# Kernel tuning notes

Hardware: AMD Instinct MI355X
Metric: run time of the kernel (lower is better)

## Reference

```python
import jax, jax.numpy as jnp
import numpy as np

EMG_SAMPLE_RATE = 2000
ROLLOUT_FREQ = 50
LEFT_CTX = 32
RIGHT_CTX = 32
NUM_POSITION_STEPS = 2000  # in EMG samples
OUT_CH = 20


def _interp_linear(x, size, align_corners):
    """x: [..., L] -> [..., size]; matches torch F.interpolate(mode='linear')."""
    L = x.shape[-1]
    if align_corners:
        src = jnp.arange(size, dtype=jnp.float32) * ((L - 1) / max(size - 1, 1))
    else:
        src = (jnp.arange(size, dtype=jnp.float32) + 0.5) * (L / size) - 0.5
        src = jnp.clip(src, 0.0, L - 1)
    lo = jnp.floor(src).astype(jnp.int32)
    hi = jnp.minimum(lo + 1, L - 1)
    w = (src - lo.astype(jnp.float32)).astype(x.dtype)
    return x[..., lo] * (1 - w) + x[..., hi] * w


def setup_inputs() -> dict:
    key = jax.random.key(0)
    ks = jax.random.split(key, 8)
    B, C, T = 32, 16, 8000
    F, K, H = 512, 65, 512
    emg = jax.random.normal(ks[0], (B, C, T), jnp.float32)
    joint_angles = jax.random.normal(ks[1], (B, OUT_CH, T), jnp.float32)
    no_ik_failure = jnp.ones((B, T), dtype=bool)
    conv_w = jax.random.normal(ks[2], (F, C, K), jnp.float32) * 0.05
    conv_b = jnp.zeros((F,), jnp.float32)
    w1 = jax.random.normal(ks[3], (F + OUT_CH, H), jnp.float32) * 0.04
    b1 = jnp.zeros((H,), jnp.float32)
    w2 = jax.random.normal(ks[4], (H, 2 * OUT_CH), jnp.float32) * 0.04
    b2 = jnp.zeros((2 * OUT_CH,), jnp.float32)
    return dict(emg=emg, joint_angles=joint_angles, no_ik_failure=no_ik_failure,
                provide_initial_pos=1, conv_w=conv_w, conv_b=conv_b,
                w1=w1, b1=b1, w2=w2, b2=b2)


def reference(emg, joint_angles, no_ik_failure, provide_initial_pos,
              conv_w, conv_b, w1, b1, w2, b2):
    B, _, T = emg.shape
    initial_pos = joint_angles[:, :, LEFT_CTX]
    if not provide_initial_pos:
        initial_pos = jnp.zeros_like(initial_pos)

    # encoder: valid Conv1d -> [B, F, T - K + 1] = [B, F, T - 64]
    feats = jax.lax.conv_general_dilated(
        emg, conv_w, window_strides=(1,), padding='VALID',
        dimension_numbers=('NCH', 'OIH', 'NCH')) + conv_b[None, :, None]

    seconds = (T - LEFT_CTX - RIGHT_CTX) / EMG_SAMPLE_RATE
    n_time = round(seconds * ROLLOUT_FREQ)          # static python int
    feats = _interp_linear(feats, n_time, align_corners=True)  # [B, F, n_time]
    num_pos_steps = round(NUM_POSITION_STEPS * (ROLLOUT_FREQ / EMG_SAMPLE_RATE))

    feats_t = jnp.transpose(feats, (2, 0, 1))  # [n_time, B, F]

    def step(prev, inp):
        x_t, t = inp
        # state_condition=True: concat previous pose prediction
        h = jax.nn.relu(jnp.concatenate([x_t, prev], axis=-1) @ w1 + b1)
        out = h @ w2 + b2                       # [B, 2*OUT_CH]
        pos, vel = out[:, :OUT_CH], out[:, OUT_CH:]
        pred = jnp.where(t < num_pos_steps, pos, prev + vel)
        return pred, pred

    _, preds = jax.lax.scan(step, initial_pos,
                            (feats_t, jnp.arange(n_time)))
    pred = jnp.transpose(preds, (1, 2, 0))  # [B, OUT_CH, n_time]

    ja = joint_angles[:, :, LEFT_CTX:T - RIGHT_CTX]
    mask = no_ik_failure[:, LEFT_CTX:T - RIGHT_CTX]
    nt = ja.shape[-1]
    pred_up = _interp_linear(pred, nt, align_corners=False)
    # nearest resample of mask to its own length is identity
    return pred_up, ja, mask
```

## Files before the change

### kernel.cpp

```cpp
#include <hip/hip_runtime.h>

#define NT   198
#define BB   32
#define CC   16
#define TT   8000
#define FF   512
#define KW   65
#define HD   512
#define OUT  20
#define CJ   (CC*KW)
#define KP   1056
#define MM   (NT*BB)
#define TOUT 7936
#define NPS  50

typedef float f4 __attribute__((ext_vector_type(4)));

#define WS_CW 0
#define WS_BX (WS_CW + KP*HD)
#define WS_X  (WS_BX + HD)
#define WS_PR (WS_X  + MM*HD)
#define WS_ET (WS_PR + MM*OUT)
#define WS_W2T (WS_ET + KP*MM)

#define ESPAN 2688
__global__ __launch_bounds__(256) void k_e2(const float* __restrict__ emg,
                                            float* __restrict__ Et) {
    __shared__ float lds_e[ESPAN];
    const int bx = blockIdx.x;
    const int bq = bx >> 4, c = bx & 15;
    const int tc = blockIdx.y;
    const int t0 = tc * 66;
    const int tid = threadIdx.x;
    const float CSTEP = 7935.0f / 197.0f;
    const int elo0 = (int)floorf((float)t0 * CSTEP);
    const float* erow = emg + (size_t)(bq * CC + c) * TT;
    for (int i = tid; i < ESPAN; i += 256) {
        int g = elo0 + i;
        lds_e[i] = erow[(g < TT) ? g : (TT - 1)];
    }
    __syncthreads();
    for (int o = tid; o < 65 * 66; o += 256) {
        int j = o / 66;
        int tl = o - j * 66;
        int t = t0 + tl;
        float src = (float)t * CSTEP;
        float fl = floorf(src);
        int lo = (int)fl;
        float w = src - fl;
        int dhi = (w > 0.f && lo < TOUT - 1) ? 1 : 0;
        int li = lo - elo0 + j;
        float v = (1.0f - w) * lds_e[li] + w * lds_e[li + dhi];
        Et[(size_t)(c * KW + j) * MM + bq * NT + t] = v;
    }
}

__global__ void k_ez(float* __restrict__ Et) {
    int r = CJ + blockIdx.x;
    int col = blockIdx.y * 256 + threadIdx.x;
    if (col < MM) Et[(size_t)r * MM + col] = 0.f;
}

__global__ __launch_bounds__(256) void k_cw2(const float* __restrict__ cwraw,
                                             const float* __restrict__ w1,
                                             float* __restrict__ CW) {
    __shared__ float As[32][68];
    __shared__ float Bs[32][68];
    const int m0 = blockIdx.x * 64;
    const int n0 = blockIdx.y * 64;
    const int tid = threadIdx.x;
    const int tx = tid & 15, ty = tid >> 4;
    const int am = tid & 63;
    const int kb8 = (tid >> 6) * 8;
    const int mrow = m0 + am;
    const int mclamp = mrow < CJ ? mrow : CJ - 1;

    f4 acc[4] = {};
    for (int k0 = 0; k0 < FF; k0 += 32) {
        __syncthreads();
        #pragma unroll
        for (int s = 0; s < 8; ++s)
            As[kb8 + s][am] = cwraw[(size_t)(k0 + kb8 + s) * CJ + mclamp];
        {
            int kb = tid >> 4, c4 = tid & 15;
            *(f4*)&Bs[kb][c4 * 4]      = *(const f4*)(w1 + (size_t)(k0 + kb) * HD + n0 + c4 * 4);
            *(f4*)&Bs[kb + 16][c4 * 4] = *(const f4*)(w1 + (size_t)(k0 + kb + 16) * HD + n0 + c4 * 4);
        }
        __syncthreads();
        #pragma unroll
        for (int kk = 0; kk < 32; ++kk) {
            f4 a = *(f4*)&As[kk][ty * 4];
            f4 bq = *(f4*)&Bs[kk][tx * 4];
            acc[0] += a[0] * bq; acc[1] += a[1] * bq;
            acc[2] += a[2] * bq; acc[3] += a[3] * bq;
        }
    }
    #pragma unroll
    for (int i = 0; i < 4; ++i) {
        int r = m0 + ty * 4 + i;
        if (r < CJ) {
            *(f4*)(CW + (size_t)r * HD + n0 + tx * 4) = acc[i];
        } else if (r < KP) {
            f4 z = {0.f, 0.f, 0.f, 0.f};
            *(f4*)(CW + (size_t)r * HD + n0 + tx * 4) = z;
        }
    }
}

__global__ void k_bx(const float* __restrict__ conv_b, const float* __restrict__ w1,
                     const float* __restrict__ b1, float* __restrict__ bX) {
    int h = threadIdx.x;
    float acc = b1[h];
    for (int f = 0; f < FF; ++f) acc += conv_b[f] * w1[f * HD + h];
    bX[h] = acc;
}

__global__ void k_w2t(const float* __restrict__ w2, float* __restrict__ w2t) {
    int q = blockIdx.x;
    int h = threadIdx.x;
    w2t[(size_t)q * HD + h] = w2[(size_t)h * (2 * OUT) + q];
}

__global__ __launch_bounds__(128) void k_x8(const float* __restrict__ Et,
                                            const float* __restrict__ CW,
                                            const float* __restrict__ bX,
                                            float* __restrict__ X0,
                                            float* __restrict__ X1) {
    __shared__ float As[32][68];
    __shared__ float Bs0[32][68];
    __shared__ float Bs1[32][68];
    const int m0 = blockIdx.x * 64;
    const int n0 = blockIdx.y * 128;
    const int kc = blockIdx.z;
    const int kbase = kc ? 512 : 0;
    const int NK = kc ? 17 : 16;
    const int tid = threadIdx.x;
    const int tm = tid >> 4;
    const int tn = tid & 15;
    const int akr = tid >> 4;
    const int ag  = tid & 15;
    const int bkr = tid >> 5;
    const int bg  = tid & 31;

    f4 acc0[8] = {}, acc1[8] = {};

    for (int kt = 0; kt < NK; ++kt) {
        const int k0 = kbase + kt * 32;
        __syncthreads();
        #pragma unroll
        for (int s = 0; s < 4; ++s) {
            f4 v = *(const f4*)(Et + (size_t)(k0 + akr + 8 * s) * MM + m0 + ag * 4);
            *(f4*)&As[akr + 8 * s][ag * 4] = v;
        }
        #pragma unroll
        for (int s = 0; s < 8; ++s) {
            int kr = bkr + 4 * s;
            f4 v = *(const f4*)(CW + (size_t)(k0 + kr) * HD + n0 + bg * 4);
            if (bg < 16) *(f4*)&Bs0[kr][bg * 4] = v;
            else         *(f4*)&Bs1[kr][(bg - 16) * 4] = v;
        }
        __syncthreads();
        #pragma unroll
        for (int kk = 0; kk < 32; ++kk) {
            f4 a0 = *(const f4*)&As[kk][tm * 8];
            f4 a1 = *(const f4*)&As[kk][tm * 8 + 4];
            f4 b0 = *(const f4*)&Bs0[kk][tn * 4];
            f4 b1 = *(const f4*)&Bs1[kk][tn * 4];
            #pragma unroll
            for (int i = 0; i < 4; ++i) {
                acc0[i]     += a0[i] * b0;  acc1[i]     += a0[i] * b1;
                acc0[i + 4] += a1[i] * b0;  acc1[i + 4] += a1[i] * b1;
            }
        }
    }

    if (kc == 0) {
        f4 bx0 = *(const f4*)(bX + n0 + tn * 4);
        f4 bx1 = *(const f4*)(bX + n0 + 64 + tn * 4);
        #pragma unroll
        for (int i = 0; i < 8; ++i) {
            size_t off = (size_t)(m0 + 8 * tm + i) * HD + n0;
            *(f4*)(X0 + off + tn * 4)      = acc0[i] + bx0;
            *(f4*)(X0 + off + 64 + tn * 4) = acc1[i] + bx1;
        }
    } else {
        #pragma unroll
        for (int i = 0; i < 8; ++i) {
            size_t off = (size_t)(m0 + 8 * tm + i) * HD + n0;
            *(f4*)(X1 + off + tn * 4)      = acc0[i];
            *(f4*)(X1 + off + 64 + tn * 4) = acc1[i];
        }
    }
}

#define DPPADD(x, ctrl) ((x) + __int_as_float(__builtin_amdgcn_mov_dpp(__float_as_int(x), (ctrl), 0xf, 0xf, true)))

#define SCAN_STEP(T, ISPOS) { \
    if (aown) { \
        int tp = (T) + 2; if (tp > NT - 1) tp = NT - 1; \
        float2 xfa = *(const float2*)(Xr0 + (size_t)tp * HD); \
        float2 xfb = *(const float2*)(Xr1 + (size_t)tp * HD); \
        float2 xf; xf.x = xfa.x + xfb.x; xf.y = xfa.y + xfb.y; \
        f4 pp[5]; \
        _Pragma("unroll") \
        for (int g = 0; g < 5; ++g) pp[g] = *(const f4*)&prev_lds[(T) & 1][g * 4]; \
        float h0 = xc.x, h1 = xc.y; \
        _Pragma("unroll") \
        for (int j = 0; j < OUT; ++j) { \
            float pj = pp[j >> 2][j & 3]; \
            h0 = fmaf(pj, w1p[j].x, h0); h1 = fmaf(pj, w1p[j].y, h1); } \
        h0 = fmaxf(h0, 0.f); h1 = fmaxf(h1, 0.f); \
        float2 hw; hw.x = h0; hw.y = h1; \
        *(float2*)&h_lds[(T) & 1][tid >> 4][(2 * tid) & 31] = hw; \
        xc = xn; xn = xf; \
    } \
    __syncthreads(); \
    f4 a = {0.f, 0.f, 0.f, 0.f}; \
    _Pragma("unroll") \
    for (int s = 0; s < 8; ++s) { \
        f4 hv = *(const f4*)&h_lds[(T) & 1][r][s * 4]; \
        a += hv * ((ISPOS) ? wqp[s] : wqv[s]); } \
    float sum = (a[0] + a[1]) + (a[2] + a[3]); \
    sum = DPPADD(sum, 0xB1);    \
    sum = DPPADD(sum, 0x4E);    \
    sum = DPPADD(sum, 0x141);   \
    sum = DPPADD(sum, 0x140);   \
    float outv = sum + ((ISPOS) ? b2p : b2v); \
    myq = (ISPOS) ? outv : (myq + outv); \
    if (r == 0) { \
        predrow[(size_t)(T) * OUT + q] = myq; \
        prev_lds[((T) + 1) & 1][q] = myq; } \
    __syncthreads(); }

__global__ __launch_bounds__(320, 1) void k_scan(
        const float* __restrict__ X0, const float* __restrict__ X1,
        const float* __restrict__ w1, const float* __restrict__ w2t,
        const float* __restrict__ b2, const float* __restrict__ jang,
        const int* __restrict__ provide, float* __restrict__ preds) {
    __shared__ float h_lds[2][16][36];
    __shared__ __align__(16) float prev_lds[2][20];
    const int b = blockIdx.x;
    const int tid = threadIdx.x;
    const int q = tid >> 4;
    const int r = tid & 15;
    const bool aown = tid < 256;

    float2 w1p[OUT];
    if (aown) {
        #pragma unroll
        for (int j = 0; j < OUT; ++j)
            w1p[j] = *(const float2*)(w1 + (size_t)(FF + j) * HD + 2 * tid);
    }
    f4 wqp[8], wqv[8];
    #pragma unroll
    for (int s = 0; s < 8; ++s) {
        wqp[s] = *(const f4*)(w2t + (size_t)q * HD + r * 32 + s * 4);
        wqv[s] = *(const f4*)(w2t + (size_t)(OUT + q) * HD + r * 32 + s * 4);
    }
    float b2p = b2[q], b2v = b2[OUT + q];

    float pvf = provide[0] ? 1.0f : 0.0f;
    float myq = pvf * jang[(size_t)(b * OUT + q) * TT + 32];
    if (r == 0) prev_lds[0][q] = myq;

    const float* Xr0 = X0 + (size_t)b * NT * HD + 2 * tid;
    const float* Xr1 = X1 + (size_t)b * NT * HD + 2 * tid;
    float* predrow = preds + (size_t)b * NT * OUT;
    float2 xc = {0.f, 0.f}, xn = {0.f, 0.f};
    if (aown) {
        float2 a0 = *(const float2*)(Xr0);
        float2 a1 = *(const float2*)(Xr1);
        xc.x = a0.x + a1.x; xc.y = a0.y + a1.y;
        float2 c0 = *(const float2*)(Xr0 + HD);
        float2 c1 = *(const float2*)(Xr1 + HD);
        xn.x = c0.x + c1.x; xn.y = c0.y + c1.y;
    }
    __syncthreads();

    for (int t = 0; t < NPS; ++t) { SCAN_STEP(t, true) }
    for (int t = NPS; t < NT; ++t) { SCAN_STEP(t, false) }
}

__global__ void k_up(const float* __restrict__ preds, float* __restrict__ outp) {
    __shared__ float row[NT];
    int rc = blockIdx.x;
    int bq = rc / OUT, ch = rc - bq * OUT;
    int tid = threadIdx.x;
    if (tid < NT) row[tid] = preds[(size_t)(bq * NT + tid) * OUT + ch];
    __syncthreads();
    const float scale = (float)NT / (float)TOUT;
    for (int i = tid; i < TOUT; i += 256) {
        float src = ((float)i + 0.5f) * scale - 0.5f;
        src = fminf(fmaxf(src, 0.0f), (float)(NT - 1));
        float fl = floorf(src);
        int lo = (int)fl;
        int hi = lo + 1; if (hi > NT - 1) hi = NT - 1;
        float w = src - fl;
        outp[(size_t)rc * TOUT + i] = row[lo] * (1.0f - w) + row[hi] * w;
    }
}

__global__ void k_ja(const float* __restrict__ jang, float* __restrict__ outp) {
    int rc = blockIdx.x;
    int tid = threadIdx.x;
    for (int i = tid; i < TOUT; i += 256)
        outp[(size_t)rc * TOUT + i] = jang[(size_t)rc * TT + 32 + i];
}

__global__ void k_mask(const unsigned char* __restrict__ m, float* __restrict__ outp) {
    int b = blockIdx.x;
    int tid = threadIdx.x;
    for (int i = tid; i < TOUT; i += 256)
        outp[(size_t)b * TOUT + i] = m[(size_t)b * TT + 32 + i] ? 1.0f : 0.0f;
}

extern "C" void kernel_launch(void* const* d_in, const int* in_sizes, int n_in,
                              void* d_out, int out_size, void* d_ws, size_t ws_size,
                              hipStream_t stream) {
    const float* emg     = (const float*)d_in[0];
    const float* jang    = (const float*)d_in[1];
    const unsigned char* msk = (const unsigned char*)d_in[2];
    const int*   provide = (const int*)d_in[3];
    const float* conv_w  = (const float*)d_in[4];
    const float* conv_b  = (const float*)d_in[5];
    const float* w1      = (const float*)d_in[6];
    const float* b1      = (const float*)d_in[7];
    const float* w2      = (const float*)d_in[8];
    const float* b2      = (const float*)d_in[9];
    float* out = (float*)d_out;
    float* ws  = (float*)d_ws;

    float* CW    = ws + WS_CW;
    float* bX    = ws + WS_BX;
    float* X0    = ws + WS_X;
    float* preds = ws + WS_PR;
    float* Et    = ws + WS_ET;
    float* w2t   = ws + WS_W2T;
    float* X1    = (float*)d_out;

    hipLaunchKernelGGL(k_e2,   dim3(BB * CC, 3), dim3(256), 0, stream, emg, Et);
    hipLaunchKernelGGL(k_ez,   dim3(KP - CJ, (MM + 255) / 256), dim3(256), 0, stream, Et);
    hipLaunchKernelGGL(k_cw2,  dim3((KP + 63) / 64, HD / 64), dim3(256), 0, stream, conv_w, w1, CW);
    hipLaunchKernelGGL(k_bx,   dim3(1), dim3(HD), 0, stream, conv_b, w1, b1, bX);
    hipLaunchKernelGGL(k_w2t,  dim3(2 * OUT), dim3(HD), 0, stream, w2, w2t);
    hipLaunchKernelGGL(k_x8,   dim3(MM / 64, HD / 128, 2), dim3(128), 0, stream, Et, CW, bX, X0, X1);
    hipLaunchKernelGGL(k_scan, dim3(BB), dim3(320), 0, stream, X0, X1, w1, w2t, b2, jang, provide, preds);
    hipLaunchKernelGGL(k_up,   dim3(BB * OUT), dim3(256), 0, stream, preds, out);
    hipLaunchKernelGGL(k_ja,   dim3(BB * OUT), dim3(256), 0, stream, jang, out + (size_t)BB * OUT * TOUT);
    hipLaunchKernelGGL(k_mask, dim3(BB), dim3(256), 0, stream, msk, out + (size_t)2 * BB * OUT * TOUT);
}
```

Measured before the change: 309.2 us.

## Split GEMM K dimension four ways and merge small and output kernels

The feature-projection GEMM now splits its reduction dimension into four chunks instead of two, writing partial sums to four buffers, three of them kept in the output region. The scan kernel sums all four partials when it reads each timestep. The bias and w2-transpose kernels are merged into one, and the three output kernels (upsample, joint-angle copy, mask) are merged into a single launch. This aims to give the GEMM more blocks for occupancy and to cut launch overhead, at the cost of extra partial-sum traffic and more loads on the serial scan's critical path.

```diff
diff --git a/kernel.cpp b/kernel.cpp
--- a/kernel.cpp
+++ b/kernel.cpp
@@ -107,33 +107,32 @@
     }
 }
 
-__global__ void k_bx(const float* __restrict__ conv_b, const float* __restrict__ w1,
-                     const float* __restrict__ b1, float* __restrict__ bX) {
+__global__ void k_small(const float* __restrict__ conv_b, const float* __restrict__ w1,
+                        const float* __restrict__ b1, const float* __restrict__ w2,
+                        float* __restrict__ bX, float* __restrict__ w2t) {
     int h = threadIdx.x;
     float acc = b1[h];
     for (int f = 0; f < FF; ++f) acc += conv_b[f] * w1[f * HD + h];
     bX[h] = acc;
-}
-
-__global__ void k_w2t(const float* __restrict__ w2, float* __restrict__ w2t) {
-    int q = blockIdx.x;
-    int h = threadIdx.x;
-    w2t[(size_t)q * HD + h] = w2[(size_t)h * (2 * OUT) + q];
-}
-
-__global__ __launch_bounds__(128) void k_x8(const float* __restrict__ Et,
+    for (int q = 0; q < 2 * OUT; ++q)
+        w2t[(size_t)q * HD + h] = w2[(size_t)h * (2 * OUT) + q];
+}
+
+__global__ __launch_bounds__(128) void k_x9(const float* __restrict__ Et,
                                             const float* __restrict__ CW,
                                             const float* __restrict__ bX,
                                             float* __restrict__ X0,
-                                            float* __restrict__ X1) {
+                                            float* __restrict__ X1,
+                                            float* __restrict__ X2,
+                                            float* __restrict__ X3) {
     __shared__ float As[32][68];
     __shared__ float Bs0[32][68];
     __shared__ float Bs1[32][68];
     const int m0 = blockIdx.x * 64;
     const int n0 = blockIdx.y * 128;
     const int kc = blockIdx.z;
-    const int kbase = kc ? 512 : 0;
-    const int NK = kc ? 17 : 16;
+    const int kbase = kc * 256;
+    const int NK = (kc == 3) ? 9 : 8;
     const int tid = threadIdx.x;
     const int tm = tid >> 4;
     const int tn = tid & 15;
@@ -174,21 +173,22 @@
         }
     }
 
+    float* Xo = (kc == 0) ? X0 : (kc == 1) ? X1 : (kc == 2) ? X2 : X3;
     if (kc == 0) {
         f4 bx0 = *(const f4*)(bX + n0 + tn * 4);
         f4 bx1 = *(const f4*)(bX + n0 + 64 + tn * 4);
         #pragma unroll
         for (int i = 0; i < 8; ++i) {
             size_t off = (size_t)(m0 + 8 * tm + i) * HD + n0;
-            *(f4*)(X0 + off + tn * 4)      = acc0[i] + bx0;
-            *(f4*)(X0 + off + 64 + tn * 4) = acc1[i] + bx1;
+            *(f4*)(Xo + off + tn * 4)      = acc0[i] + bx0;
+            *(f4*)(Xo + off + 64 + tn * 4) = acc1[i] + bx1;
         }
     } else {
         #pragma unroll
         for (int i = 0; i < 8; ++i) {
             size_t off = (size_t)(m0 + 8 * tm + i) * HD + n0;
-            *(f4*)(X1 + off + tn * 4)      = acc0[i];
-            *(f4*)(X1 + off + 64 + tn * 4) = acc1[i];
+            *(f4*)(Xo + off + tn * 4)      = acc0[i];
+            *(f4*)(Xo + off + 64 + tn * 4) = acc1[i];
         }
     }
 }
@@ -200,7 +200,11 @@
         int tp = (T) + 2; if (tp > NT - 1) tp = NT - 1; \
         float2 xfa = *(const float2*)(Xr0 + (size_t)tp * HD); \
         float2 xfb = *(const float2*)(Xr1 + (size_t)tp * HD); \
-        float2 xf; xf.x = xfa.x + xfb.x; xf.y = xfa.y + xfb.y; \
+        float2 xfc = *(const float2*)(Xr2 + (size_t)tp * HD); \
+        float2 xfd = *(const float2*)(Xr3 + (size_t)tp * HD); \
+        float2 xf; \
+        xf.x = (xfa.x + xfb.x) + (xfc.x + xfd.x); \
+        xf.y = (xfa.y + xfb.y) + (xfc.y + xfd.y); \
         f4 pp[5]; \
         _Pragma("unroll") \
         for (int g = 0; g < 5; ++g) pp[g] = *(const f4*)&prev_lds[(T) & 1][g * 4]; \
@@ -234,6 +238,7 @@
 
 __global__ __launch_bounds__(320, 1) void k_scan(
         const float* __restrict__ X0, const float* __restrict__ X1,
+        const float* __restrict__ X2, const float* __restrict__ X3,
         const float* __restrict__ w1, const float* __restrict__ w2t,
         const float* __restrict__ b2, const float* __restrict__ jang,
         const int* __restrict__ provide, float* __restrict__ preds) {
@@ -265,15 +270,23 @@
 
     const float* Xr0 = X0 + (size_t)b * NT * HD + 2 * tid;
     const float* Xr1 = X1 + (size_t)b * NT * HD + 2 * tid;
+    const float* Xr2 = X2 + (size_t)b * NT * HD + 2 * tid;
+    const float* Xr3 = X3 + (size_t)b * NT * HD + 2 * tid;
     float* predrow = preds + (size_t)b * NT * OUT;
     float2 xc = {0.f, 0.f}, xn = {0.f, 0.f};
     if (aown) {
         float2 a0 = *(const float2*)(Xr0);
         float2 a1 = *(const float2*)(Xr1);
-        xc.x = a0.x + a1.x; xc.y = a0.y + a1.y;
+        float2 a2 = *(const float2*)(Xr2);
+        float2 a3 = *(const float2*)(Xr3);
+        xc.x = (a0.x + a1.x) + (a2.x + a3.x);
+        xc.y = (a0.y + a1.y) + (a2.y + a3.y);
         float2 c0 = *(const float2*)(Xr0 + HD);
         float2 c1 = *(const float2*)(Xr1 + HD);
-        xn.x = c0.x + c1.x; xn.y = c0.y + c1.y;
+        float2 c2 = *(const float2*)(Xr2 + HD);
+        float2 c3 = *(const float2*)(Xr3 + HD);
+        xn.x = (c0.x + c1.x) + (c2.x + c3.x);
+        xn.y = (c0.y + c1.y) + (c2.y + c3.y);
     }
     __syncthreads();
 
@@ -281,37 +294,39 @@
     for (int t = NPS; t < NT; ++t) { SCAN_STEP(t, false) }
 }
 
-__global__ void k_up(const float* __restrict__ preds, float* __restrict__ outp) {
+__global__ __launch_bounds__(256) void k_out(const float* __restrict__ preds,
+                                             const float* __restrict__ jang,
+                                             const unsigned char* __restrict__ m,
+                                             float* __restrict__ outp) {
     __shared__ float row[NT];
-    int rc = blockIdx.x;
-    int bq = rc / OUT, ch = rc - bq * OUT;
-    int tid = threadIdx.x;
-    if (tid < NT) row[tid] = preds[(size_t)(bq * NT + tid) * OUT + ch];
-    __syncthreads();
-    const float scale = (float)NT / (float)TOUT;
-    for (int i = tid; i < TOUT; i += 256) {
-        float src = ((float)i + 0.5f) * scale - 0.5f;
-        src = fminf(fmaxf(src, 0.0f), (float)(NT - 1));
-        float fl = floorf(src);
-        int lo = (int)fl;
-        int hi = lo + 1; if (hi > NT - 1) hi = NT - 1;
-        float w = src - fl;
-        outp[(size_t)rc * TOUT + i] = row[lo] * (1.0f - w) + row[hi] * w;
-    }
-}
-
-__global__ void k_ja(const float* __restrict__ jang, float* __restrict__ outp) {
-    int rc = blockIdx.x;
-    int tid = threadIdx.x;
-    for (int i = tid; i < TOUT; i += 256)
-        outp[(size_t)rc * TOUT + i] = jang[(size_t)rc * TT + 32 + i];
-}
-
-__global__ void k_mask(const unsigned char* __restrict__ m, float* __restrict__ outp) {
-    int b = blockIdx.x;
-    int tid = threadIdx.x;
-    for (int i = tid; i < TOUT; i += 256)
-        outp[(size_t)b * TOUT + i] = m[(size_t)b * TT + 32 + i] ? 1.0f : 0.0f;
+    const int bid = blockIdx.x;
+    const int tid = threadIdx.x;
+    if (bid < BB * OUT) {
+        int rc = bid;
+        int bq = rc / OUT, ch = rc - bq * OUT;
+        if (tid < NT) row[tid] = preds[(size_t)(bq * NT + tid) * OUT + ch];
+        __syncthreads();
+        const float scale = (float)NT / (float)TOUT;
+        for (int i = tid; i < TOUT; i += 256) {
+            float src = ((float)i + 0.5f) * scale - 0.5f;
+            src = fminf(fmaxf(src, 0.0f), (float)(NT - 1));
+            float fl = floorf(src);
+            int lo = (int)fl;
+            int hi = lo + 1; if (hi > NT - 1) hi = NT - 1;
+            float w = src - fl;
+            outp[(size_t)rc * TOUT + i] = row[lo] * (1.0f - w) + row[hi] * w;
+        }
+    } else if (bid < 2 * BB * OUT) {
+        int rc = bid - BB * OUT;
+        float* op = outp + (size_t)BB * OUT * TOUT;
+        for (int i = tid; i < TOUT; i += 256)
+            op[(size_t)rc * TOUT + i] = jang[(size_t)rc * TT + 32 + i];
+    } else {
+        int b = bid - 2 * BB * OUT;
+        float* op = outp + (size_t)2 * BB * OUT * TOUT;
+        for (int i = tid; i < TOUT; i += 256)
+            op[(size_t)b * TOUT + i] = m[(size_t)b * TT + 32 + i] ? 1.0f : 0.0f;
+    }
 }
 
 extern "C" void kernel_launch(void* const* d_in, const int* in_sizes, int n_in,
@@ -336,16 +351,18 @@
     float* preds = ws + WS_PR;
     float* Et    = ws + WS_ET;
     float* w2t   = ws + WS_W2T;
-    float* X1    = (float*)d_out;
+    float* X1    = out;
+    float* X2    = out + (size_t)MM * HD;
+    float* X3    = out + (size_t)2 * MM * HD;
 
     hipLaunchKernelGGL(k_e2,   dim3(BB * CC, 3), dim3(256), 0, stream, emg, Et);
     hipLaunchKernelGGL(k_ez,   dim3(KP - CJ, (MM + 255) / 256), dim3(256), 0, stream, Et);
     hipLaunchKernelGGL(k_cw2,  dim3((KP + 63) / 64, HD / 64), dim3(256), 0, stream, conv_w, w1, CW);
-    hipLaunchKernelGGL(k_bx,   dim3(1), dim3(HD), 0, stream, conv_b, w1, b1, bX);
-    hipLaunchKernelGGL(k_w2t,  dim3(2 * OUT), dim3(HD), 0, stream, w2, w2t);
-    hipLaunchKernelGGL(k_x8,   dim3(MM / 64, HD / 128, 2), dim3(128), 0, stream, Et, CW, bX, X0, X1);
-    hipLaunchKernelGGL(k_scan, dim3(BB), dim3(320), 0, stream, X0, X1, w1, w2t, b2, jang, provide, preds);
-    hipLaunchKernelGGL(k_up,   dim3(BB * OUT), dim3(256), 0, stream, preds, out);
-    hipLaunchKernelGGL(k_ja,   dim3(BB * OUT), dim3(256), 0, stream, jang, out + (size_t)BB * OUT * TOUT);
-    hipLaunchKernelGGL(k_mask, dim3(BB), dim3(256), 0, stream, msk, out + (size_t)2 * BB * OUT * TOUT);
-}
+    hipLaunchKernelGGL(k_small, dim3(1), dim3(HD), 0, stream, conv_b, w1, b1, w2, bX, w2t);
+    hipLaunchKernelGGL(k_x9,   dim3(MM / 64, HD / 128, 4), dim3(128), 0, stream,
+                       Et, CW, bX, X0, X1, X2, X3);
+    hipLaunchKernelGGL(k_scan, dim3(BB), dim3(320), 0, stream,
+                       X0, X1, X2, X3, w1, w2t, b2, jang, provide, preds);
+    hipLaunchKernelGGL(k_out,  dim3(2 * BB * OUT + BB), dim3(256), 0, stream,
+                       preds, jang, msk, out);
+}
```

After: 317.1 us. +2.6%, slower.
